# Kernel tuning notes

Hardware: AMD Instinct MI355X
Metric: run time of the kernel (lower is better)

## Reference

```python
import jax, jax.numpy as jnp
import numpy as np
from jax import lax


def fps(xyz, npoint, init_far):
    # Faithful farthest-point sampling: sequential loop over npoint iterations.
    B, N, _ = xyz.shape
    bidx = jnp.arange(B)

    def step(carry, _):
        dist, far = carry
        c = xyz[bidx, far]                       # (B,3) current centroid
        d = jnp.sum((xyz - c[:, None, :]) ** 2, -1)  # (B,N)
        dist = jnp.minimum(dist, d)
        return (dist, jnp.argmax(dist, -1)), far     # emit index BEFORE update, as in torch

    init = (jnp.full((B, N), 1e10, xyz.dtype), init_far)
    _, cent = lax.scan(step, init, None, length=npoint)  # (npoint, B)
    return cent.T                                         # (B, npoint)


def gather_pts(feat, idx):
    # feat (B,N,C), idx (B,K) -> (B,K,C)
    return jnp.take_along_axis(feat, idx[..., None], axis=1)


def setup_inputs() -> dict:
    key = jax.random.key(0)
    ks = jax.random.split(key, 12)
    B, N = 128, 500

    def w(k, o, i):
        return jax.random.normal(k, (o, i), jnp.float32) * 0.02

    z = lambda o: jnp.zeros((o,), jnp.float32)
    return {
        "x": jax.random.normal(ks[0], (B, N, 3), jnp.float32),
        "conf_W": w(ks[1], 1, 3),   "conf_b": z(1),
        "w1": w(ks[2], 64, 4),      "b1": z(64),
        "w2": w(ks[3], 256, 64),    "b2": z(256),
        "pc1_W": w(ks[4], 256, 256),"pc1_b": z(256),
        "w3": w(ks[5], 256, 259),   "b3": z(256),
        "w4": w(ks[6], 384, 256),   "b4": z(384),
        "pc2_W": w(ks[7], 384, 384),"pc2_b": z(384),
        "w5": w(ks[8], 384, 387),   "b5": z(384),
        "w6": w(ks[9], 512, 384),   "b6": z(512),
        "model_weights": 0,
        "init_far1": jax.random.randint(ks[10], (B,), 0, N),
        "init_far2": jax.random.randint(ks[11], (B,), 0, N),
    }


def reference(x, conf_W, conf_b, w1, b1, w2, b2, pc1_W, pc1_b,
              w3, b3, w4, b4, pc2_W, pc2_b, w5, b5, w6, b6,
              model_weights, init_far1, init_far2):
    relu = jax.nn.relu
    lin = lambda h, W, b: h @ W.T + b

    # ConfidenceScorePredictor: per-point sigmoid score (1 channel)
    conf = jax.nn.sigmoid(lin(x, conf_W, conf_b))            # (B,N,1)
    feat = jnp.concatenate([conf, x], -1)                    # (B,N,4)

    l2 = relu(lin(relu(lin(feat, w1, b1)), w2, b2))          # (B,N,256)
    l3 = lin(l2, pc1_W, pc1_b)                               # Conv1d k=1 == per-point linear

    idx1 = fps(x, 500, init_far1)                            # (B,500)
    nf1 = jnp.concatenate([gather_pts(l3, idx1), gather_pts(x, idx1)], -1)  # (B,500,259)

    l5 = relu(lin(relu(lin(nf1, w3, b3)), w4, b4))           # (B,500,384)
    l6 = lin(l5, pc2_W, pc2_b)                               # (B,500,384)

    idx2 = fps(x, 1000, init_far2)                           # (B,1000), indices < 500
    nf2 = jnp.concatenate([gather_pts(l6, idx2), gather_pts(x, idx2)], -1)  # (B,1000,387)

    l8 = relu(lin(relu(lin(nf2, w5, b5)), w6, b6))           # (B,1000,512)
    return jnp.max(l8, axis=1)                               # MaxPool1d(k=1000) -> (B,512)
```

## Files before the change

### kernel.cpp

```cpp
#include <hip/hip_runtime.h>

typedef unsigned short u16;
typedef short bf16x8 __attribute__((ext_vector_type(8)));
typedef float f32x4 __attribute__((ext_vector_type(4)));
typedef unsigned short us8 __attribute__((ext_vector_type(8)));
typedef unsigned long long u64;

__device__ __forceinline__ float bf2f(u16 u) {
  return __uint_as_float(((unsigned)u) << 16);
}
__device__ __forceinline__ u16 f2bf(float f) {
  unsigned u = __float_as_uint(f);
  u += 0x7fffu + ((u >> 16) & 1u);
  return (u16)(u >> 16);
}
__device__ __forceinline__ float rlf(float v, int l) {
  return __uint_as_float((unsigned)__builtin_amdgcn_readlane(__float_as_int(v), l));
}
__device__ __forceinline__ void gload16(const u16* g, u16* l) {
  __builtin_amdgcn_global_load_lds(
      (const __attribute__((address_space(1))) void*)g,
      (__attribute__((address_space(3))) void*)l, 16, 0, 0);
}

#define M_AB 64000
#define M_C 65536

#define OFF_ARENA_B 49152000u
#define OFF_IDX1 149815296u
#define OFF_FPSD 150071296u
#define OFF_FPSI 150333440u
#define OFF_WB   150583296u

template <int CTRL>
__device__ __forceinline__ float dppmaxf(float v) {
  int s = __builtin_amdgcn_update_dpp(0, __float_as_int(v), CTRL, 0xF, 0xF, true);
  return fmaxf(v, __uint_as_float((unsigned)s));
}

__device__ void fps_seg(const float4* cpt, int* out, const int* init1,
                        float* dstate, int* fstate, int b, int t0, int tcnt,
                        int lane) {
  float px[8], py[8], pz[8], dist[8];
  int base = lane * 8;
#pragma unroll
  for (int j = 0; j < 8; ++j) {
    int p = base + j;
    float4 c = cpt[p < 500 ? p : 0];
    px[j] = c.x; py[j] = c.y; pz[j] = c.z;
  }
  int fidx;
  if (t0 == 0) {
#pragma unroll
    for (int j = 0; j < 8; ++j) dist[j] = 1e10f;
    fidx = init1[b];
  } else {
#pragma unroll
    for (int j = 0; j < 8; ++j) dist[j] = dstate[(b * 64 + lane) * 8 + j];
    fidx = fstate[b];
  }
  float4 c0 = cpt[fidx];
  float cx = c0.x, cy = c0.y, cz = c0.z;

  int tend = t0 + tcnt;
  for (int t = t0; t < tend; ++t) {
    if (lane == 0) out[t] = fidx;
    if (t == 499) return;
#pragma unroll
    for (int j = 0; j < 8; ++j) {
      float dx = __fsub_rn(px[j], cx);
      float dy = __fsub_rn(py[j], cy);
      float dz = __fsub_rn(pz[j], cz);
      float d = __fadd_rn(__fadd_rn(__fmul_rn(dx, dx), __fmul_rn(dy, dy)),
                          __fmul_rn(dz, dz));
      dist[j] = fminf(dist[j], d);
    }
    float m01 = fmaxf(dist[0], dist[1]), m23 = fmaxf(dist[2], dist[3]);
    float m45 = fmaxf(dist[4], dist[5]), m67 = fmaxf(dist[6], dist[7]);
    float lm = fmaxf(fmaxf(m01, m23), fmaxf(m45, m67));
    lm = dppmaxf<0x111>(lm);
    lm = dppmaxf<0x112>(lm);
    lm = dppmaxf<0x114>(lm);
    lm = dppmaxf<0x118>(lm);
    lm = dppmaxf<0x142>(lm);
    lm = dppmaxf<0x143>(lm);
    float mf = rlf(lm, 63);
    int sel = 8;
    float sx = 0.f, sy = 0.f, sz = 0.f;
#pragma unroll
    for (int j = 7; j >= 0; --j) {
      bool hit = (dist[j] == mf);
      sel = hit ? j : sel;
      sx = hit ? px[j] : sx;
      sy = hit ? py[j] : sy;
      sz = hit ? pz[j] : sz;
    }
    u64 mask = __ballot(sel != 8);
    int li = (int)__ffsll(mask) - 1;
    fidx = li * 8 + __builtin_amdgcn_readlane(sel, li);
    cx = rlf(sx, li);
    cy = rlf(sy, li);
    cz = rlf(sz, li);
  }
#pragma unroll
  for (int j = 0; j < 8; ++j) dstate[(b * 64 + lane) * 8 + j] = dist[j];
  if (lane == 0) fstate[b] = fidx;
}

#define SMEM_BYTES (16384 * 2 + 1024)

__device__ __forceinline__ void gemm_body(
    const u16* __restrict__ A, int lda, const float* __restrict__ X,
    const int* __restrict__ idx, int mode, const u16* __restrict__ Wb,
    int ldw, const float* __restrict__ bias, u16* __restrict__ C, int ldc,
    int Kp, int N, int act, float* __restrict__ outf, int bx, int by,
    char* smem, int t) {
  u16* lA = (u16*)smem;
  u16* lB = (u16*)(smem + 16384);
  float* red = (float*)(smem + 32768);

  const int m0 = bx * 128, n0 = by * 128;
  const int w = t >> 6, lane = t & 63;
  const int mrow = lane & 15, quad = lane >> 4;
  const int wm = w >> 1, wn = w & 1;

  const int lrow8 = lane >> 3;
  const int sseg = (lane & 7) ^ lrow8;

  const u16* arow[4];
  const u16* wrow[4];
#pragma unroll
  for (int i = 0; i < 4; ++i) {
    int gr = m0 + w * 32 + i * 8 + lrow8;
    if (mode == 4) {
      int b = gr >> 9;
      int p = gr & 511;
      int pe = (p < 500) ? p : 0;
      int s = idx[b * 500 + pe];
      arow[i] = A + ((size_t)b * 500 + s) * lda;
    } else {
      arow[i] = A + (size_t)gr * lda;
    }
    wrow[i] = Wb + (size_t)(n0 + w * 32 + i * 8 + lrow8) * ldw;
  }
  const int fr = t >> 1;
  const int fs0 = (t & 1) * 4;
  const u16* faptr;
  const float* fxptr = nullptr;
  {
    int gr = m0 + fr;
    if (mode == 4) {
      int b = gr >> 9;
      int p = gr & 511;
      int pe = (p < 500) ? p : 0;
      int s = idx[b * 500 + pe];
      faptr = A + ((size_t)b * 500 + s) * lda;
      fxptr = X + ((size_t)b * 500 + pe) * 3;
    } else {
      faptr = A + (size_t)gr * lda;
      if (mode == 2) fxptr = X + (size_t)gr * 3;
    }
  }
  const int kfull = lda & ~63;

  f32x4 acc[4][4];
  const f32x4 fz = {0.f, 0.f, 0.f, 0.f};
#pragma unroll
  for (int i = 0; i < 4; ++i)
#pragma unroll
    for (int j = 0; j < 4; ++j) acc[i][j] = fz;

  for (int k0 = 0; k0 < Kp; k0 += 64) {
    __syncthreads();
#pragma unroll
    for (int i = 0; i < 4; ++i)
      gload16(wrow[i] + k0 + sseg * 8, lB + (w * 32 + i * 8) * 64);
    if (k0 < kfull) {
#pragma unroll
      for (int i = 0; i < 4; ++i)
        gload16(arow[i] + k0 + sseg * 8, lA + (w * 32 + i * 8) * 64);
    } else {
#pragma unroll
      for (int s4 = 0; s4 < 4; ++s4) {
        int seg = fs0 + s4;
        us8 v = {0, 0, 0, 0, 0, 0, 0, 0};
        int kb = k0 + seg * 8;
#pragma unroll
        for (int j = 0; j < 8; ++j) {
          int k = kb + j;
          u16 vv = 0;
          if (k < lda) vv = faptr[k];
          else if (mode != 0 && k < lda + 3) vv = f2bf(fxptr[k - lda]);
          v[j] = vv;
        }
        *(us8*)(lA + fr * 64 + (seg ^ (fr & 7)) * 8) = v;
      }
    }
    __syncthreads();

#pragma unroll
    for (int kh = 0; kh < 2; ++kh) {
      bf16x8 af[4], bfv[4];
#pragma unroll
      for (int mi = 0; mi < 4; ++mi) {
        int r = wm * 64 + mi * 16 + mrow;
        af[mi] = *(const bf16x8*)(lA + r * 64 + ((kh * 4 + quad) ^ (r & 7)) * 8);
      }
#pragma unroll
      for (int ni = 0; ni < 4; ++ni) {
        int r = wn * 64 + ni * 16 + mrow;
        bfv[ni] = *(const bf16x8*)(lB + r * 64 + ((kh * 4 + quad) ^ (r & 7)) * 8);
      }
#pragma unroll
      for (int mi = 0; mi < 4; ++mi)
#pragma unroll
        for (int ni = 0; ni < 4; ++ni)
          acc[mi][ni] = __builtin_amdgcn_mfma_f32_16x16x32_bf16(
              af[mi], bfv[ni], acc[mi][ni], 0, 0, 0);
    }
  }

  if (act < 2) {
#pragma unroll
    for (int ni = 0; ni < 4; ++ni) {
      int col = n0 + wn * 64 + ni * 16 + mrow;
      if (col >= N) continue;
      float bv = bias[col];
#pragma unroll
      for (int mi = 0; mi < 4; ++mi)
#pragma unroll
        for (int r = 0; r < 4; ++r) {
          int grow = m0 + wm * 64 + mi * 16 + quad * 4 + r;
          float v = acc[mi][ni][r] + bv;
          if (act == 1) v = fmaxf(v, 0.f);
          C[(size_t)grow * ldc + col] = f2bf(v);
        }
    }
  } else {
#pragma unroll
    for (int ni = 0; ni < 4; ++ni) {
      int col = n0 + wn * 64 + ni * 16 + mrow;
      float bv = (col < N) ? bias[col] : 0.f;
      float mx = 0.f;
#pragma unroll
      for (int mi = 0; mi < 4; ++mi)
#pragma unroll
        for (int r = 0; r < 4; ++r) {
          int grow = m0 + wm * 64 + mi * 16 + quad * 4 + r;
          float v = fmaxf(acc[mi][ni][r] + bv, 0.f);
          if ((grow & 511) < 500) mx = fmaxf(mx, v);
        }
      mx = fmaxf(mx, __shfl_xor(mx, 16, 64));
      mx = fmaxf(mx, __shfl_xor(mx, 32, 64));
      if (quad == 0) red[wm * 128 + wn * 64 + ni * 16 + mrow] = mx;
    }
    __syncthreads();
    if (t < 128) {
      int col = n0 + t;
      if (col < N) {
        float m = fmaxf(red[t], red[128 + t]);
        int b = m0 >> 9;
        atomicMax((unsigned*)&outf[b * 512 + col], __float_as_uint(m));
      }
    }
  }
}

__global__ __launch_bounds__(256) void gemm_mfma(
    const u16* __restrict__ A, int lda, const float* __restrict__ X,
    const int* __restrict__ idx, int mode, const u16* __restrict__ Wb,
    int ldw, const float* __restrict__ bias, u16* __restrict__ C, int ldc,
    int Kp, int N, int act, float* __restrict__ outf) {
  __shared__ __align__(16) char smem[SMEM_BYTES];
  gemm_body(A, lda, X, idx, mode, Wb, ldw, bias, C, ldc, Kp, N, act, outf,
            blockIdx.x, blockIdx.y, smem, threadIdx.x);
}

__global__ __launch_bounds__(256) void gemm_fps(
    const u16* __restrict__ A, int lda, const float* __restrict__ X,
    int mode, const u16* __restrict__ Wb, int ldw,
    const float* __restrict__ bias, u16* __restrict__ C, int ldc, int Kp,
    int N, int act, int gx, const float* __restrict__ x,
    const int* __restrict__ init1, int* __restrict__ idx1,
    float* __restrict__ dstate, int* __restrict__ fstate, int t0, int tcnt) {
  __shared__ __align__(16) char smem[SMEM_BYTES];
  int bid = blockIdx.x;
  int t = threadIdx.x;
  if (bid < 128) {
    int b = bid;
    float4* cpt = (float4*)smem;
    const float* xb = x + (size_t)b * 1500;
    for (int p = t; p < 500; p += 256)
      cpt[p] = make_float4(xb[p * 3], xb[p * 3 + 1], xb[p * 3 + 2], 0.f);
    __syncthreads();
    if (t < 64)
      fps_seg(cpt, idx1 + b * 500, init1, dstate, fstate, b, t0, tcnt, t);
  } else {
    int g = bid - 128;
    int by = g / gx, bx = g - by * gx;
    gemm_body(A, lda, X, nullptr, mode, Wb, ldw, bias, C, ldc, Kp, N, act,
              nullptr, bx, by, smem, t);
  }
}

struct PrepArgs {
  const float* wsrc[8];
  u16* wdst[8];
  int wN[8], wK[8], wKp[8];
  int wstart[9];
};

__global__ __launch_bounds__(256) void prep_kernel(
    PrepArgs pa, const float* __restrict__ x, const float* __restrict__ cW,
    const float* __restrict__ cb, u16* __restrict__ feat,
    float* __restrict__ outf, const int* __restrict__ init1,
    int* __restrict__ idx1, float* __restrict__ dstate,
    int* __restrict__ fstate, int tcnt) {
  __shared__ float4 cpt[512];
  int bid = blockIdx.x;
  int t = threadIdx.x;
  if (bid < 128) {
    int b = bid;
    const float* xb = x + (size_t)b * 1500;
    for (int p = t; p < 500; p += 256)
      cpt[p] = make_float4(xb[p * 3], xb[p * 3 + 1], xb[p * 3 + 2], 0.f);
    __syncthreads();
    if (t < 64) fps_seg(cpt, idx1 + b * 500, init1, dstate, fstate, b, 0, tcnt, t);
    return;
  }
  int i = (bid - 128) * 256 + t;
  int S = pa.wstart[8];
  if (i < S) {
    int w = 0;
#pragma unroll
    for (int j = 1; j < 8; ++j)
      if (i >= pa.wstart[j]) w = j;
    int local = i - pa.wstart[w];
    int Kp = pa.wKp[w];
    int n = local / Kp, k = local - n * Kp;
    pa.wdst[w][local] =
        (n < pa.wN[w] && k < pa.wK[w]) ? f2bf(pa.wsrc[w][n * pa.wK[w] + k]) : (u16)0;
  } else if (i < S + 65536) {
    outf[i - S] = 0.f;
  } else {
    int r = i - S - 65536;
    if (r < M_AB) {
      float x0 = x[r * 3], x1 = x[r * 3 + 1], x2 = x[r * 3 + 2];
      float z = x0 * cW[0] + x1 * cW[1] + x2 * cW[2] + cb[0];
      float conf = 1.0f / (1.0f + expf(-z));
      feat[r * 4 + 0] = f2bf(conf);
      feat[r * 4 + 1] = f2bf(x0);
      feat[r * 4 + 2] = f2bf(x1);
      feat[r * 4 + 3] = f2bf(x2);
    }
  }
}

extern "C" void kernel_launch(void* const* d_in, const int* in_sizes, int n_in,
                              void* d_out, int out_size, void* d_ws,
                              size_t ws_size, hipStream_t stream) {
  const float* x      = (const float*)d_in[0];
  const float* conf_W = (const float*)d_in[1];
  const float* conf_b = (const float*)d_in[2];
  const float* w1     = (const float*)d_in[3];
  const float* b1     = (const float*)d_in[4];
  const float* w2     = (const float*)d_in[5];
  const float* b2     = (const float*)d_in[6];
  const float* pc1_W  = (const float*)d_in[7];
  const float* pc1_b  = (const float*)d_in[8];
  const float* w3     = (const float*)d_in[9];
  const float* b3     = (const float*)d_in[10];
  const float* w4     = (const float*)d_in[11];
  const float* b4     = (const float*)d_in[12];
  const float* pc2_W  = (const float*)d_in[13];
  const float* pc2_b  = (const float*)d_in[14];
  const float* w5     = (const float*)d_in[15];
  const float* b5     = (const float*)d_in[16];
  const float* w6     = (const float*)d_in[17];
  const float* b6     = (const float*)d_in[18];
  const int* init1    = (const int*)d_in[20];

  char* ws = (char*)d_ws;
  u16* feat = (u16*)(ws + 0);
  u16* l2b  = (u16*)(ws + 0);
  u16* l4b  = (u16*)(ws + 0);
  u16* l6u  = (u16*)(ws + 0);
  u16* l1b  = (u16*)(ws + OFF_ARENA_B);
  u16* l3b  = (u16*)(ws + OFF_ARENA_B);
  u16* l5b  = (u16*)(ws + OFF_ARENA_B);
  u16* l7b  = (u16*)(ws + OFF_ARENA_B);
  int* idx1 = (int*)(ws + OFF_IDX1);
  float* dstate = (float*)(ws + OFF_FPSD);
  int* fstate   = (int*)(ws + OFF_FPSI);
  u16* wb   = (u16*)(ws + OFF_WB);
  float* outf = (float*)d_out;

  PrepArgs pa;
  const float* srcs[8] = {w1, w2, pc1_W, w3, w4, pc2_W, w5, w6};
  int Ns[8]  = {64, 256, 256, 256, 384, 384, 384, 512};
  int Nps[8] = {128, 256, 256, 256, 384, 384, 384, 512};
  int Ks[8]  = {4, 64, 256, 259, 256, 384, 387, 384};
  int Kps[8] = {64, 64, 256, 320, 256, 384, 448, 384};
  u16* WBp[8];
  int cum = 0;
  for (int i = 0; i < 8; ++i) {
    pa.wsrc[i] = srcs[i];
    pa.wdst[i] = WBp[i] = wb + cum;
    pa.wN[i] = Ns[i];
    pa.wK[i] = Ks[i];
    pa.wKp[i] = Kps[i];
    pa.wstart[i] = cum;
    cum += Nps[i] * Kps[i];
  }
  pa.wstart[8] = cum;
  int total = cum + 65536 + M_AB;

  prep_kernel<<<128 + (total + 255) / 256, 256, 0, stream>>>(
      pa, x, conf_W, conf_b, feat, outf, init1, idx1, dstate, fstate, 60);
  gemm_fps<<<128 + 500, 256, 0, stream>>>(feat, 4, nullptr, 0, WBp[0], 64,
      b1, l1b, 64, 64, 64, 1, 500, x, init1, idx1, dstate, fstate, 60, 40);
  gemm_fps<<<128 + 1000, 256, 0, stream>>>(l1b, 64, nullptr, 0, WBp[1], 64,
      b2, l2b, 256, 64, 256, 1, 500, x, init1, idx1, dstate, fstate, 100, 50);
  gemm_fps<<<128 + 1000, 256, 0, stream>>>(l2b, 256, nullptr, 0, WBp[2], 256,
      pc1_b, l3b, 256, 256, 256, 0, 500, x, init1, idx1, dstate, fstate, 150, 70);
  gemm_fps<<<128 + 1000, 256, 0, stream>>>(l3b, 256, x, 2, WBp[3], 320,
      b3, l4b, 256, 320, 256, 1, 500, x, init1, idx1, dstate, fstate, 220, 85);
  gemm_fps<<<128 + 1500, 256, 0, stream>>>(l4b, 256, nullptr, 0, WBp[4], 256,
      b4, l5b, 384, 256, 384, 1, 500, x, init1, idx1, dstate, fstate, 305, 90);
  gemm_fps<<<128 + 1500, 256, 0, stream>>>(l5b, 384, nullptr, 0, WBp[5], 384,
      pc2_b, l6u, 384, 384, 384, 0, 500, x, init1, idx1, dstate, fstate, 395, 105);
  gemm_mfma<<<dim3(512, 3), 256, 0, stream>>>(l6u, 384, x, idx1, 4,
      WBp[6], 448, b5, l7b, 384, 448, 384, 1, nullptr);
  gemm_mfma<<<dim3(512, 4), 256, 0, stream>>>(l7b, 384, nullptr, nullptr, 0,
      WBp[7], 384, b6, nullptr, 0, 384, 512, 2, outf);
}
```

Baseline: 400.0 us.

## Load GEMM fragments directly from global and interleave two FPS batches per wave

The GEMM body drops its LDS staging (global_load_lds plus barriers) and has each lane load its MFMA A/B fragments straight from global memory with a one-step register prefetch, stepping K by 32. The FPS side blocks now process two batches per wave, interleaving two independent dependency chains to hide latency and halving the number of FPS blocks. The GEMM change removes barriers and LDS traffic but gives up cross-wave reuse of tiles through shared memory, so global/L2 traffic per block rises. The FPS change adds register pressure and makes each FPS block's serial work longer.

```diff
diff --git a/kernel.cpp b/kernel.cpp
--- a/kernel.cpp
+++ b/kernel.cpp
@@ -3,7 +3,6 @@
 typedef unsigned short u16;
 typedef short bf16x8 __attribute__((ext_vector_type(8)));
 typedef float f32x4 __attribute__((ext_vector_type(4)));
-typedef unsigned short us8 __attribute__((ext_vector_type(8)));
 typedef unsigned long long u64;
 
 __device__ __forceinline__ float bf2f(u16 u) {
@@ -16,11 +15,6 @@
 }
 __device__ __forceinline__ float rlf(float v, int l) {
   return __uint_as_float((unsigned)__builtin_amdgcn_readlane(__float_as_int(v), l));
-}
-__device__ __forceinline__ void gload16(const u16* g, u16* l) {
-  __builtin_amdgcn_global_load_lds(
-      (const __attribute__((address_space(1))) void*)g,
-      (__attribute__((address_space(3))) void*)l, 16, 0, 0);
 }
 
 #define M_AB 64000
@@ -38,130 +32,147 @@
   return fmaxf(v, __uint_as_float((unsigned)s));
 }
 
-__device__ void fps_seg(const float4* cpt, int* out, const int* init1,
-                        float* dstate, int* fstate, int b, int t0, int tcnt,
-                        int lane) {
-  float px[8], py[8], pz[8], dist[8];
+__device__ void fps_seg2(const float4* cpt0, const float4* cpt1, int* out0,
+                         int* out1, const int* init1, float* dstate,
+                         int* fstate, int b0, int b1, int t0, int tcnt,
+                         int lane) {
+  float px0[8], py0[8], pz0[8], d0[8];
+  float px1[8], py1[8], pz1[8], d1[8];
   int base = lane * 8;
 #pragma unroll
   for (int j = 0; j < 8; ++j) {
     int p = base + j;
-    float4 c = cpt[p < 500 ? p : 0];
-    px[j] = c.x; py[j] = c.y; pz[j] = c.z;
-  }
-  int fidx;
+    int pe = p < 500 ? p : 0;
+    float4 c = cpt0[pe];
+    px0[j] = c.x; py0[j] = c.y; pz0[j] = c.z;
+    c = cpt1[pe];
+    px1[j] = c.x; py1[j] = c.y; pz1[j] = c.z;
+  }
+  int f0, f1;
   if (t0 == 0) {
 #pragma unroll
-    for (int j = 0; j < 8; ++j) dist[j] = 1e10f;
-    fidx = init1[b];
+    for (int j = 0; j < 8; ++j) { d0[j] = 1e10f; d1[j] = 1e10f; }
+    f0 = init1[b0];
+    f1 = init1[b1];
   } else {
 #pragma unroll
-    for (int j = 0; j < 8; ++j) dist[j] = dstate[(b * 64 + lane) * 8 + j];
-    fidx = fstate[b];
-  }
-  float4 c0 = cpt[fidx];
-  float cx = c0.x, cy = c0.y, cz = c0.z;
+    for (int j = 0; j < 8; ++j) {
+      d0[j] = dstate[(b0 * 64 + lane) * 8 + j];
+      d1[j] = dstate[(b1 * 64 + lane) * 8 + j];
+    }
+    f0 = fstate[b0];
+    f1 = fstate[b1];
+  }
+  float4 cc = cpt0[f0];
+  float cx0 = cc.x, cy0 = cc.y, cz0 = cc.z;
+  cc = cpt1[f1];
+  float cx1 = cc.x, cy1 = cc.y, cz1 = cc.z;
 
   int tend = t0 + tcnt;
   for (int t = t0; t < tend; ++t) {
-    if (lane == 0) out[t] = fidx;
+    if (lane == 0) { out0[t] = f0; out1[t] = f1; }
     if (t == 499) return;
 #pragma unroll
     for (int j = 0; j < 8; ++j) {
-      float dx = __fsub_rn(px[j], cx);
-      float dy = __fsub_rn(py[j], cy);
-      float dz = __fsub_rn(pz[j], cz);
-      float d = __fadd_rn(__fadd_rn(__fmul_rn(dx, dx), __fmul_rn(dy, dy)),
-                          __fmul_rn(dz, dz));
-      dist[j] = fminf(dist[j], d);
-    }
-    float m01 = fmaxf(dist[0], dist[1]), m23 = fmaxf(dist[2], dist[3]);
-    float m45 = fmaxf(dist[4], dist[5]), m67 = fmaxf(dist[6], dist[7]);
-    float lm = fmaxf(fmaxf(m01, m23), fmaxf(m45, m67));
-    lm = dppmaxf<0x111>(lm);
-    lm = dppmaxf<0x112>(lm);
-    lm = dppmaxf<0x114>(lm);
-    lm = dppmaxf<0x118>(lm);
-    lm = dppmaxf<0x142>(lm);
-    lm = dppmaxf<0x143>(lm);
-    float mf = rlf(lm, 63);
-    int sel = 8;
-    float sx = 0.f, sy = 0.f, sz = 0.f;
+      float dx = __fsub_rn(px0[j], cx0);
+      float dy = __fsub_rn(py0[j], cy0);
+      float dz = __fsub_rn(pz0[j], cz0);
+      float dd = __fadd_rn(__fadd_rn(__fmul_rn(dx, dx), __fmul_rn(dy, dy)),
+                           __fmul_rn(dz, dz));
+      d0[j] = fminf(d0[j], dd);
+      dx = __fsub_rn(px1[j], cx1);
+      dy = __fsub_rn(py1[j], cy1);
+      dz = __fsub_rn(pz1[j], cz1);
+      dd = __fadd_rn(__fadd_rn(__fmul_rn(dx, dx), __fmul_rn(dy, dy)),
+                     __fmul_rn(dz, dz));
+      d1[j] = fminf(d1[j], dd);
+    }
+    float lm0 = fmaxf(fmaxf(fmaxf(d0[0], d0[1]), fmaxf(d0[2], d0[3])),
+                      fmaxf(fmaxf(d0[4], d0[5]), fmaxf(d0[6], d0[7])));
+    float lm1 = fmaxf(fmaxf(fmaxf(d1[0], d1[1]), fmaxf(d1[2], d1[3])),
+                      fmaxf(fmaxf(d1[4], d1[5]), fmaxf(d1[6], d1[7])));
+    lm0 = dppmaxf<0x111>(lm0); lm1 = dppmaxf<0x111>(lm1);
+    lm0 = dppmaxf<0x112>(lm0); lm1 = dppmaxf<0x112>(lm1);
+    lm0 = dppmaxf<0x114>(lm0); lm1 = dppmaxf<0x114>(lm1);
+    lm0 = dppmaxf<0x118>(lm0); lm1 = dppmaxf<0x118>(lm1);
+    lm0 = dppmaxf<0x142>(lm0); lm1 = dppmaxf<0x142>(lm1);
+    lm0 = dppmaxf<0x143>(lm0); lm1 = dppmaxf<0x143>(lm1);
+    float mf0 = rlf(lm0, 63), mf1 = rlf(lm1, 63);
+    int s0 = 8, s1 = 8;
+    float sx0 = 0, sy0 = 0, sz0 = 0, sx1 = 0, sy1 = 0, sz1 = 0;
 #pragma unroll
     for (int j = 7; j >= 0; --j) {
-      bool hit = (dist[j] == mf);
-      sel = hit ? j : sel;
-      sx = hit ? px[j] : sx;
-      sy = hit ? py[j] : sy;
-      sz = hit ? pz[j] : sz;
-    }
-    u64 mask = __ballot(sel != 8);
-    int li = (int)__ffsll(mask) - 1;
-    fidx = li * 8 + __builtin_amdgcn_readlane(sel, li);
-    cx = rlf(sx, li);
-    cy = rlf(sy, li);
-    cz = rlf(sz, li);
-  }
-#pragma unroll
-  for (int j = 0; j < 8; ++j) dstate[(b * 64 + lane) * 8 + j] = dist[j];
-  if (lane == 0) fstate[b] = fidx;
-}
-
-#define SMEM_BYTES (16384 * 2 + 1024)
+      bool h0 = (d0[j] == mf0);
+      s0 = h0 ? j : s0; sx0 = h0 ? px0[j] : sx0;
+      sy0 = h0 ? py0[j] : sy0; sz0 = h0 ? pz0[j] : sz0;
+      bool h1 = (d1[j] == mf1);
+      s1 = h1 ? j : s1; sx1 = h1 ? px1[j] : sx1;
+      sy1 = h1 ? py1[j] : sy1; sz1 = h1 ? pz1[j] : sz1;
+    }
+    u64 m0 = __ballot(s0 != 8);
+    int li0 = (int)__ffsll(m0) - 1;
+    f0 = li0 * 8 + __builtin_amdgcn_readlane(s0, li0);
+    cx0 = rlf(sx0, li0); cy0 = rlf(sy0, li0); cz0 = rlf(sz0, li0);
+    u64 m1 = __ballot(s1 != 8);
+    int li1 = (int)__ffsll(m1) - 1;
+    f1 = li1 * 8 + __builtin_amdgcn_readlane(s1, li1);
+    cx1 = rlf(sx1, li1); cy1 = rlf(sy1, li1); cz1 = rlf(sz1, li1);
+  }
+#pragma unroll
+  for (int j = 0; j < 8; ++j) {
+    dstate[(b0 * 64 + lane) * 8 + j] = d0[j];
+    dstate[(b1 * 64 + lane) * 8 + j] = d1[j];
+  }
+  if (lane == 0) { fstate[b0] = f0; fstate[b1] = f1; }
+}
+
+__device__ __forceinline__ bf16x8 load_afrag(const u16* ar, int c, int lda,
+                                             const float* xr, int mode) {
+  if (c + 8 <= lda) return *(const bf16x8*)(ar + c);
+  bf16x8 v = {0, 0, 0, 0, 0, 0, 0, 0};
+#pragma unroll
+  for (int j = 0; j < 8; ++j) {
+    int k = c + j;
+    u16 vv = 0;
+    if (k < lda) vv = ar[k];
+    else if (mode != 0 && k < lda + 3) vv = f2bf(xr[k - lda]);
+    v[j] = (short)vv;
+  }
+  return v;
+}
 
 __device__ __forceinline__ void gemm_body(
     const u16* __restrict__ A, int lda, const float* __restrict__ X,
     const int* __restrict__ idx, int mode, const u16* __restrict__ Wb,
     int ldw, const float* __restrict__ bias, u16* __restrict__ C, int ldc,
     int Kp, int N, int act, float* __restrict__ outf, int bx, int by,
-    char* smem, int t) {
-  u16* lA = (u16*)smem;
-  u16* lB = (u16*)(smem + 16384);
-  float* red = (float*)(smem + 32768);
-
+    float* red, int t) {
   const int m0 = bx * 128, n0 = by * 128;
   const int w = t >> 6, lane = t & 63;
   const int mrow = lane & 15, quad = lane >> 4;
   const int wm = w >> 1, wn = w & 1;
 
-  const int lrow8 = lane >> 3;
-  const int sseg = (lane & 7) ^ lrow8;
-
-  const u16* arow[4];
-  const u16* wrow[4];
-#pragma unroll
-  for (int i = 0; i < 4; ++i) {
-    int gr = m0 + w * 32 + i * 8 + lrow8;
+  const u16* ar[4];
+  const float* xr[4];
+#pragma unroll
+  for (int mi = 0; mi < 4; ++mi) {
+    int gr = m0 + wm * 64 + mi * 16 + mrow;
     if (mode == 4) {
       int b = gr >> 9;
       int p = gr & 511;
       int pe = (p < 500) ? p : 0;
       int s = idx[b * 500 + pe];
-      arow[i] = A + ((size_t)b * 500 + s) * lda;
+      ar[mi] = A + ((size_t)b * 500 + s) * lda;
+      xr[mi] = X + ((size_t)b * 500 + pe) * 3;
     } else {
-      arow[i] = A + (size_t)gr * lda;
-    }
-    wrow[i] = Wb + (size_t)(n0 + w * 32 + i * 8 + lrow8) * ldw;
-  }
-  const int fr = t >> 1;
-  const int fs0 = (t & 1) * 4;
-  const u16* faptr;
-  const float* fxptr = nullptr;
-  {
-    int gr = m0 + fr;
-    if (mode == 4) {
-      int b = gr >> 9;
-      int p = gr & 511;
-      int pe = (p < 500) ? p : 0;
-      int s = idx[b * 500 + pe];
-      faptr = A + ((size_t)b * 500 + s) * lda;
-      fxptr = X + ((size_t)b * 500 + pe) * 3;
-    } else {
-      faptr = A + (size_t)gr * lda;
-      if (mode == 2) fxptr = X + (size_t)gr * 3;
-    }
-  }
-  const int kfull = lda & ~63;
+      ar[mi] = A + (size_t)gr * lda;
+      xr[mi] = X + (size_t)gr * 3;
+    }
+  }
+  const u16* wr[4];
+#pragma unroll
+  for (int ni = 0; ni < 4; ++ni)
+    wr[ni] = Wb + (size_t)(n0 + wn * 64 + ni * 16 + mrow) * ldw;
 
   f32x4 acc[4][4];
   const f32x4 fz = {0.f, 0.f, 0.f, 0.f};
@@ -170,54 +181,31 @@
 #pragma unroll
     for (int j = 0; j < 4; ++j) acc[i][j] = fz;
 
-  for (int k0 = 0; k0 < Kp; k0 += 64) {
-    __syncthreads();
-#pragma unroll
-    for (int i = 0; i < 4; ++i)
-      gload16(wrow[i] + k0 + sseg * 8, lB + (w * 32 + i * 8) * 64);
-    if (k0 < kfull) {
-#pragma unroll
-      for (int i = 0; i < 4; ++i)
-        gload16(arow[i] + k0 + sseg * 8, lA + (w * 32 + i * 8) * 64);
-    } else {
-#pragma unroll
-      for (int s4 = 0; s4 < 4; ++s4) {
-        int seg = fs0 + s4;
-        us8 v = {0, 0, 0, 0, 0, 0, 0, 0};
-        int kb = k0 + seg * 8;
-#pragma unroll
-        for (int j = 0; j < 8; ++j) {
-          int k = kb + j;
-          u16 vv = 0;
-          if (k < lda) vv = faptr[k];
-          else if (mode != 0 && k < lda + 3) vv = f2bf(fxptr[k - lda]);
-          v[j] = vv;
-        }
-        *(us8*)(lA + fr * 64 + (seg ^ (fr & 7)) * 8) = v;
-      }
-    }
-    __syncthreads();
-
-#pragma unroll
-    for (int kh = 0; kh < 2; ++kh) {
-      bf16x8 af[4], bfv[4];
-#pragma unroll
-      for (int mi = 0; mi < 4; ++mi) {
-        int r = wm * 64 + mi * 16 + mrow;
-        af[mi] = *(const bf16x8*)(lA + r * 64 + ((kh * 4 + quad) ^ (r & 7)) * 8);
-      }
-#pragma unroll
-      for (int ni = 0; ni < 4; ++ni) {
-        int r = wn * 64 + ni * 16 + mrow;
-        bfv[ni] = *(const bf16x8*)(lB + r * 64 + ((kh * 4 + quad) ^ (r & 7)) * 8);
-      }
-#pragma unroll
-      for (int mi = 0; mi < 4; ++mi)
-#pragma unroll
-        for (int ni = 0; ni < 4; ++ni)
-          acc[mi][ni] = __builtin_amdgcn_mfma_f32_16x16x32_bf16(
-              af[mi], bfv[ni], acc[mi][ni], 0, 0, 0);
-    }
+  const int cq = quad * 8;
+  bf16x8 a_cur[4], b_cur[4];
+#pragma unroll
+  for (int mi = 0; mi < 4; ++mi)
+    a_cur[mi] = load_afrag(ar[mi], cq, lda, xr[mi], mode);
+#pragma unroll
+  for (int ni = 0; ni < 4; ++ni) b_cur[ni] = *(const bf16x8*)(wr[ni] + cq);
+
+  for (int k0 = 0; k0 < Kp; k0 += 32) {
+    int kn = (k0 + 32 < Kp) ? (k0 + 32) : k0;
+    int cn = kn + cq;
+    bf16x8 a_nxt[4], b_nxt[4];
+#pragma unroll
+    for (int mi = 0; mi < 4; ++mi)
+      a_nxt[mi] = load_afrag(ar[mi], cn, lda, xr[mi], mode);
+#pragma unroll
+    for (int ni = 0; ni < 4; ++ni) b_nxt[ni] = *(const bf16x8*)(wr[ni] + cn);
+#pragma unroll
+    for (int mi = 0; mi < 4; ++mi)
+#pragma unroll
+      for (int ni = 0; ni < 4; ++ni)
+        acc[mi][ni] = __builtin_amdgcn_mfma_f32_16x16x32_bf16(
+            a_cur[mi], b_cur[ni], acc[mi][ni], 0, 0, 0);
+#pragma unroll
+    for (int i = 0; i < 4; ++i) { a_cur[i] = a_nxt[i]; b_cur[i] = b_nxt[i]; }
   }
 
   if (act < 2) {
@@ -271,35 +259,40 @@
     const int* __restrict__ idx, int mode, const u16* __restrict__ Wb,
     int ldw, const float* __restrict__ bias, u16* __restrict__ C, int ldc,
     int Kp, int N, int act, float* __restrict__ outf) {
-  __shared__ __align__(16) char smem[SMEM_BYTES];
+  __shared__ __align__(16) float red[256];
   gemm_body(A, lda, X, idx, mode, Wb, ldw, bias, C, ldc, Kp, N, act, outf,
-            blockIdx.x, blockIdx.y, smem, threadIdx.x);
+            blockIdx.x, blockIdx.y, red, threadIdx.x);
 }
 
 __global__ __launch_bounds__(256) void gemm_fps(
-    const u16* __restrict__ A, int lda, const float* __restrict__ X,
-    int mode, const u16* __restrict__ Wb, int ldw,
-    const float* __restrict__ bias, u16* __restrict__ C, int ldc, int Kp,
-    int N, int act, int gx, const float* __restrict__ x,
-    const int* __restrict__ init1, int* __restrict__ idx1,
-    float* __restrict__ dstate, int* __restrict__ fstate, int t0, int tcnt) {
-  __shared__ __align__(16) char smem[SMEM_BYTES];
+    const u16* __restrict__ A, int lda, const float* __restrict__ X, int mode,
+    const u16* __restrict__ Wb, int ldw, const float* __restrict__ bias,
+    u16* __restrict__ C, int ldc, int Kp, int N, int act, int gx,
+    const float* __restrict__ x, const int* __restrict__ init1,
+    int* __restrict__ idx1, float* __restrict__ dstate,
+    int* __restrict__ fstate, int t0, int tcnt) {
+  __shared__ __align__(16) float4 smem[1024];
   int bid = blockIdx.x;
   int t = threadIdx.x;
-  if (bid < 128) {
-    int b = bid;
-    float4* cpt = (float4*)smem;
-    const float* xb = x + (size_t)b * 1500;
-    for (int p = t; p < 500; p += 256)
-      cpt[p] = make_float4(xb[p * 3], xb[p * 3 + 1], xb[p * 3 + 2], 0.f);
+  if (bid < 64) {
+    int b0 = bid * 2, b1 = bid * 2 + 1;
+    float4* cpt0 = smem;
+    float4* cpt1 = smem + 512;
+    const float* xb0 = x + (size_t)b0 * 1500;
+    const float* xb1 = x + (size_t)b1 * 1500;
+    for (int p = t; p < 500; p += 256) {
+      cpt0[p] = make_float4(xb0[p * 3], xb0[p * 3 + 1], xb0[p * 3 + 2], 0.f);
+      cpt1[p] = make_float4(xb1[p * 3], xb1[p * 3 + 1], xb1[p * 3 + 2], 0.f);
+    }
     __syncthreads();
     if (t < 64)
-      fps_seg(cpt, idx1 + b * 500, init1, dstate, fstate, b, t0, tcnt, t);
+      fps_seg2(cpt0, cpt1, idx1 + b0 * 500, idx1 + b1 * 500, init1, dstate,
+               fstate, b0, b1, t0, tcnt, t);
   } else {
-    int g = bid - 128;
+    int g = bid - 64;
     int by = g / gx, bx = g - by * gx;
     gemm_body(A, lda, X, nullptr, mode, Wb, ldw, bias, C, ldc, Kp, N, act,
-              nullptr, bx, by, smem, t);
+              nullptr, bx, by, (float*)smem, t);
   }
 }
 
@@ -316,19 +309,24 @@
     float* __restrict__ outf, const int* __restrict__ init1,
     int* __restrict__ idx1, float* __restrict__ dstate,
     int* __restrict__ fstate, int tcnt) {
-  __shared__ float4 cpt[512];
+  __shared__ float4 cpt[1024];
   int bid = blockIdx.x;
   int t = threadIdx.x;
-  if (bid < 128) {
-    int b = bid;
-    const float* xb = x + (size_t)b * 1500;
-    for (int p = t; p < 500; p += 256)
-      cpt[p] = make_float4(xb[p * 3], xb[p * 3 + 1], xb[p * 3 + 2], 0.f);
+  if (bid < 64) {
+    int b0 = bid * 2, b1 = bid * 2 + 1;
+    const float* xb0 = x + (size_t)b0 * 1500;
+    const float* xb1 = x + (size_t)b1 * 1500;
+    for (int p = t; p < 500; p += 256) {
+      cpt[p] = make_float4(xb0[p * 3], xb0[p * 3 + 1], xb0[p * 3 + 2], 0.f);
+      cpt[512 + p] = make_float4(xb1[p * 3], xb1[p * 3 + 1], xb1[p * 3 + 2], 0.f);
+    }
     __syncthreads();
-    if (t < 64) fps_seg(cpt, idx1 + b * 500, init1, dstate, fstate, b, 0, tcnt, t);
+    if (t < 64)
+      fps_seg2(cpt, cpt + 512, idx1 + b0 * 500, idx1 + b1 * 500, init1,
+               dstate, fstate, b0, b1, 0, tcnt, t);
     return;
   }
-  int i = (bid - 128) * 256 + t;
+  int i = (bid - 64) * 256 + t;
   int S = pa.wstart[8];
   if (i < S) {
     int w = 0;
@@ -415,19 +413,19 @@
   pa.wstart[8] = cum;
   int total = cum + 65536 + M_AB;
 
-  prep_kernel<<<128 + (total + 255) / 256, 256, 0, stream>>>(
+  prep_kernel<<<64 + (total + 255) / 256, 256, 0, stream>>>(
       pa, x, conf_W, conf_b, feat, outf, init1, idx1, dstate, fstate, 60);
-  gemm_fps<<<128 + 500, 256, 0, stream>>>(feat, 4, nullptr, 0, WBp[0], 64,
+  gemm_fps<<<64 + 500, 256, 0, stream>>>(feat, 4, x, 0, WBp[0], 64,
       b1, l1b, 64, 64, 64, 1, 500, x, init1, idx1, dstate, fstate, 60, 40);
-  gemm_fps<<<128 + 1000, 256, 0, stream>>>(l1b, 64, nullptr, 0, WBp[1], 64,
+  gemm_fps<<<64 + 1000, 256, 0, stream>>>(l1b, 64, x, 0, WBp[1], 64,
       b2, l2b, 256, 64, 256, 1, 500, x, init1, idx1, dstate, fstate, 100, 50);
-  gemm_fps<<<128 + 1000, 256, 0, stream>>>(l2b, 256, nullptr, 0, WBp[2], 256,
+  gemm_fps<<<64 + 1000, 256, 0, stream>>>(l2b, 256, x, 0, WBp[2], 256,
       pc1_b, l3b, 256, 256, 256, 0, 500, x, init1, idx1, dstate, fstate, 150, 70);
-  gemm_fps<<<128 + 1000, 256, 0, stream>>>(l3b, 256, x, 2, WBp[3], 320,
+  gemm_fps<<<64 + 1000, 256, 0, stream>>>(l3b, 256, x, 2, WBp[3], 320,
       b3, l4b, 256, 320, 256, 1, 500, x, init1, idx1, dstate, fstate, 220, 85);
-  gemm_fps<<<128 + 1500, 256, 0, stream>>>(l4b, 256, nullptr, 0, WBp[4], 256,
+  gemm_fps<<<64 + 1500, 256, 0, stream>>>(l4b, 256, x, 0, WBp[4], 256,
       b4, l5b, 384, 256, 384, 1, 500, x, init1, idx1, dstate, fstate, 305, 90);
-  gemm_fps<<<128 + 1500, 256, 0, stream>>>(l5b, 384, nullptr, 0, WBp[5], 384,
+  gemm_fps<<<64 + 1500, 256, 0, stream>>>(l5b, 384, x, 0, WBp[5], 384,
       pc2_b, l6u, 384, 384, 384, 0, 500, x, init1, idx1, dstate, fstate, 395, 105);
   gemm_mfma<<<dim3(512, 3), 256, 0, stream>>>(l6u, 384, x, idx1, 4,
       WBp[6], 448, b5, l7b, 384, 448, 384, 1, nullptr);
```

Result: slower. 655.5 us (+63.9%).

## Pack four FPS batches per block and fuse first linear layer into prep

Applied to the files above, without the earlier changes.

The first layer (4→64 linear + ReLU) is now computed directly in the prep kernel on scalar FMAs, which removes one gemm_fps launch and the intermediate feat buffer. FPS work is packed as four batches per block, one per wavefront, instead of one wave per block, so 32 blocks carry the FPS segments instead of 128. The FPS iteration counts per segment are redistributed across the remaining six launches. This frees CUs for GEMM tiles and cuts one launch, at the cost of four waves contending in one block and the prep kernel doing more scalar work per point.

```diff
diff --git a/kernel.cpp b/kernel.cpp
--- a/kernel.cpp
+++ b/kernel.cpp
@@ -105,6 +105,24 @@
 #pragma unroll
   for (int j = 0; j < 8; ++j) dstate[(b * 64 + lane) * 8 + j] = dist[j];
   if (lane == 0) fstate[b] = fidx;
+}
+
+__device__ __forceinline__ void fps_block4(float4* cpt, const float* x,
+                                           const int* init1, int* idx1,
+                                           float* dstate, int* fstate,
+                                           int bid, int t0, int tcnt, int t) {
+#pragma unroll
+  for (int wv = 0; wv < 4; ++wv) {
+    const float* xb = x + (size_t)(bid * 4 + wv) * 1500;
+    for (int p = t; p < 500; p += 256)
+      cpt[wv * 512 + p] =
+          make_float4(xb[p * 3], xb[p * 3 + 1], xb[p * 3 + 2], 0.f);
+  }
+  __syncthreads();
+  int wv = t >> 6;
+  int b = bid * 4 + wv;
+  fps_seg(cpt + wv * 512, idx1 + b * 500, init1, dstate, fstate, b, t0, tcnt,
+          t & 63);
 }
 
 #define SMEM_BYTES (16384 * 2 + 1024)
@@ -277,26 +295,19 @@
 }
 
 __global__ __launch_bounds__(256) void gemm_fps(
-    const u16* __restrict__ A, int lda, const float* __restrict__ X,
-    int mode, const u16* __restrict__ Wb, int ldw,
-    const float* __restrict__ bias, u16* __restrict__ C, int ldc, int Kp,
-    int N, int act, int gx, const float* __restrict__ x,
-    const int* __restrict__ init1, int* __restrict__ idx1,
-    float* __restrict__ dstate, int* __restrict__ fstate, int t0, int tcnt) {
+    const u16* __restrict__ A, int lda, const float* __restrict__ X, int mode,
+    const u16* __restrict__ Wb, int ldw, const float* __restrict__ bias,
+    u16* __restrict__ C, int ldc, int Kp, int N, int act, int gx,
+    const float* __restrict__ x, const int* __restrict__ init1,
+    int* __restrict__ idx1, float* __restrict__ dstate,
+    int* __restrict__ fstate, int t0, int tcnt) {
   __shared__ __align__(16) char smem[SMEM_BYTES];
   int bid = blockIdx.x;
   int t = threadIdx.x;
-  if (bid < 128) {
-    int b = bid;
-    float4* cpt = (float4*)smem;
-    const float* xb = x + (size_t)b * 1500;
-    for (int p = t; p < 500; p += 256)
-      cpt[p] = make_float4(xb[p * 3], xb[p * 3 + 1], xb[p * 3 + 2], 0.f);
-    __syncthreads();
-    if (t < 64)
-      fps_seg(cpt, idx1 + b * 500, init1, dstate, fstate, b, t0, tcnt, t);
+  if (bid < 32) {
+    fps_block4((float4*)smem, x, init1, idx1, dstate, fstate, bid, t0, tcnt, t);
   } else {
-    int g = bid - 128;
+    int g = bid - 32;
     int by = g / gx, bx = g - by * gx;
     gemm_body(A, lda, X, nullptr, mode, Wb, ldw, bias, C, ldc, Kp, N, act,
               nullptr, bx, by, smem, t);
@@ -304,36 +315,32 @@
 }
 
 struct PrepArgs {
-  const float* wsrc[8];
-  u16* wdst[8];
-  int wN[8], wK[8], wKp[8];
-  int wstart[9];
+  const float* wsrc[7];
+  u16* wdst[7];
+  int wN[7], wK[7], wKp[7];
+  int wstart[8];
 };
 
 __global__ __launch_bounds__(256) void prep_kernel(
     PrepArgs pa, const float* __restrict__ x, const float* __restrict__ cW,
-    const float* __restrict__ cb, u16* __restrict__ feat,
+    const float* __restrict__ cb, const float* __restrict__ w1,
+    const float* __restrict__ b1, u16* __restrict__ l1,
     float* __restrict__ outf, const int* __restrict__ init1,
     int* __restrict__ idx1, float* __restrict__ dstate,
     int* __restrict__ fstate, int tcnt) {
-  __shared__ float4 cpt[512];
+  __shared__ __align__(16) float4 cpt[2048];
   int bid = blockIdx.x;
   int t = threadIdx.x;
-  if (bid < 128) {
-    int b = bid;
-    const float* xb = x + (size_t)b * 1500;
-    for (int p = t; p < 500; p += 256)
-      cpt[p] = make_float4(xb[p * 3], xb[p * 3 + 1], xb[p * 3 + 2], 0.f);
-    __syncthreads();
-    if (t < 64) fps_seg(cpt, idx1 + b * 500, init1, dstate, fstate, b, 0, tcnt, t);
+  if (bid < 32) {
+    fps_block4(cpt, x, init1, idx1, dstate, fstate, bid, 0, tcnt, t);
     return;
   }
-  int i = (bid - 128) * 256 + t;
-  int S = pa.wstart[8];
+  int i = (bid - 32) * 256 + t;
+  int S = pa.wstart[7];
   if (i < S) {
     int w = 0;
 #pragma unroll
-    for (int j = 1; j < 8; ++j)
+    for (int j = 1; j < 7; ++j)
       if (i >= pa.wstart[j]) w = j;
     int local = i - pa.wstart[w];
     int Kp = pa.wKp[w];
@@ -348,10 +355,21 @@
       float x0 = x[r * 3], x1 = x[r * 3 + 1], x2 = x[r * 3 + 2];
       float z = x0 * cW[0] + x1 * cW[1] + x2 * cW[2] + cb[0];
       float conf = 1.0f / (1.0f + expf(-z));
-      feat[r * 4 + 0] = f2bf(conf);
-      feat[r * 4 + 1] = f2bf(x0);
-      feat[r * 4 + 2] = f2bf(x1);
-      feat[r * 4 + 3] = f2bf(x2);
+      u16* dst = l1 + (size_t)r * 64;
+#pragma unroll
+      for (int n8 = 0; n8 < 64; n8 += 8) {
+        us8 v;
+#pragma unroll
+        for (int j = 0; j < 8; ++j) {
+          const float* wr = w1 + (n8 + j) * 4;
+          float a = fmaf(conf, wr[0], b1[n8 + j]);
+          a = fmaf(x0, wr[1], a);
+          a = fmaf(x1, wr[2], a);
+          a = fmaf(x2, wr[3], a);
+          v[j] = f2bf(fmaxf(a, 0.f));
+        }
+        *(us8*)(dst + n8) = v;
+      }
     }
   }
 }
@@ -381,7 +399,6 @@
   const int* init1    = (const int*)d_in[20];
 
   char* ws = (char*)d_ws;
-  u16* feat = (u16*)(ws + 0);
   u16* l2b  = (u16*)(ws + 0);
   u16* l4b  = (u16*)(ws + 0);
   u16* l6u  = (u16*)(ws + 0);
@@ -396,41 +413,38 @@
   float* outf = (float*)d_out;
 
   PrepArgs pa;
-  const float* srcs[8] = {w1, w2, pc1_W, w3, w4, pc2_W, w5, w6};
-  int Ns[8]  = {64, 256, 256, 256, 384, 384, 384, 512};
-  int Nps[8] = {128, 256, 256, 256, 384, 384, 384, 512};
-  int Ks[8]  = {4, 64, 256, 259, 256, 384, 387, 384};
-  int Kps[8] = {64, 64, 256, 320, 256, 384, 448, 384};
-  u16* WBp[8];
+  const float* srcs[7] = {w2, pc1_W, w3, w4, pc2_W, w5, w6};
+  int Ns[7]  = {256, 256, 256, 384, 384, 384, 512};
+  int Ks[7]  = {64, 256, 259, 256, 384, 387, 384};
+  int Kps[7] = {64, 256, 320, 256, 384, 448, 384};
+  u16* WBp[7];
   int cum = 0;
-  for (int i = 0; i < 8; ++i) {
+  for (int i = 0; i < 7; ++i) {
     pa.wsrc[i] = srcs[i];
     pa.wdst[i] = WBp[i] = wb + cum;
     pa.wN[i] = Ns[i];
     pa.wK[i] = Ks[i];
     pa.wKp[i] = Kps[i];
     pa.wstart[i] = cum;
-    cum += Nps[i] * Kps[i];
-  }
-  pa.wstart[8] = cum;
+    cum += Ns[i] * Kps[i];
+  }
+  pa.wstart[7] = cum;
   int total = cum + 65536 + M_AB;
 
-  prep_kernel<<<128 + (total + 255) / 256, 256, 0, stream>>>(
-      pa, x, conf_W, conf_b, feat, outf, init1, idx1, dstate, fstate, 60);
-  gemm_fps<<<128 + 500, 256, 0, stream>>>(feat, 4, nullptr, 0, WBp[0], 64,
-      b1, l1b, 64, 64, 64, 1, 500, x, init1, idx1, dstate, fstate, 60, 40);
-  gemm_fps<<<128 + 1000, 256, 0, stream>>>(l1b, 64, nullptr, 0, WBp[1], 64,
-      b2, l2b, 256, 64, 256, 1, 500, x, init1, idx1, dstate, fstate, 100, 50);
-  gemm_fps<<<128 + 1000, 256, 0, stream>>>(l2b, 256, nullptr, 0, WBp[2], 256,
-      pc1_b, l3b, 256, 256, 256, 0, 500, x, init1, idx1, dstate, fstate, 150, 70);
-  gemm_fps<<<128 + 1000, 256, 0, stream>>>(l3b, 256, x, 2, WBp[3], 320,
-      b3, l4b, 256, 320, 256, 1, 500, x, init1, idx1, dstate, fstate, 220, 85);
-  gemm_fps<<<128 + 1500, 256, 0, stream>>>(l4b, 256, nullptr, 0, WBp[4], 256,
-      b4, l5b, 384, 256, 384, 1, 500, x, init1, idx1, dstate, fstate, 305, 90);
-  gemm_fps<<<128 + 1500, 256, 0, stream>>>(l5b, 384, nullptr, 0, WBp[5], 384,
-      pc2_b, l6u, 384, 384, 384, 0, 500, x, init1, idx1, dstate, fstate, 395, 105);
+  prep_kernel<<<32 + (total + 255) / 256, 256, 0, stream>>>(
+      pa, x, conf_W, conf_b, w1, b1, l1b, outf, init1, idx1, dstate, fstate, 40);
+  gemm_fps<<<32 + 1000, 256, 0, stream>>>(l1b, 64, x, 0, WBp[0], 64,
+      b2, l2b, 256, 64, 256, 1, 500, x, init1, idx1, dstate, fstate, 40, 50);
+  gemm_fps<<<32 + 1000, 256, 0, stream>>>(l2b, 256, x, 0, WBp[1], 256,
+      pc1_b, l3b, 256, 256, 256, 0, 500, x, init1, idx1, dstate, fstate, 90, 70);
+  gemm_fps<<<32 + 1000, 256, 0, stream>>>(l3b, 256, x, 2, WBp[2], 320,
+      b3, l4b, 256, 320, 256, 1, 500, x, init1, idx1, dstate, fstate, 160, 100);
+  gemm_fps<<<32 + 1500, 256, 0, stream>>>(l4b, 256, x, 0, WBp[3], 256,
+      b4, l5b, 384, 256, 384, 1, 500, x, init1, idx1, dstate, fstate, 260, 110);
+  gemm_fps<<<32 + 1500, 256, 0, stream>>>(l5b, 384, x, 0, WBp[4], 384,
+      pc2_b, l6u, 384, 384, 384, 0, 500, x, init1, idx1, dstate, fstate, 370, 130);
   gemm_mfma<<<dim3(512, 3), 256, 0, stream>>>(l6u, 384, x, idx1, 4,
-      WBp[6], 448, b5, l7b, 384, 448, 384, 1, nullptr);
+      WBp[5], 448, b5, l7b, 384, 448, 384, 1, nullptr);
   gemm_mfma<<<dim3(512, 4), 256, 0, stream>>>(l7b, 384, nullptr, nullptr, 0,
-      WBp[7], 384, b6, nullptr, 0, 384, 512, 2, outf);
-}
+      WBp[6], 384, b6, nullptr, 0, 384, 512, 2, outf);
+}
```

Result: slower. 413.1 us (+3.3%).
